# Kernel tuning notes

Hardware: AMD Instinct MI355X
Metric: run time of the kernel (lower is better)

The kernel has to match this reference:

```python
import jax, jax.numpy as jnp
import numpy as np

B, M, C = 8, 8192, 256   # batch, seeds, seed feature dim
F = 128                  # vote feature dim
P, K = 256, 32           # proposals, samples per group
CA, NCLS = 256, 10       # aggregated feat dim, classes
RADIUS = 0.3


def _lin(x, w, b):
    # 1x1 conv == pointwise linear; w: (out, in)
    return jnp.einsum('...c,oc->...o', x, w) + b


def _bnrelu(x, s, t):
    # eval-mode BatchNorm folded to per-channel affine, then ReLU
    return jnp.maximum(x * s + t, 0.0)


def _fps(xyz, npoint):
    # farthest point sampling; deterministic start at index 0
    Bb, N, _ = xyz.shape
    bidx = jnp.arange(Bb)

    def step(carry, _):
        distance, farthest = carry
        centroid = xyz[bidx, farthest][:, None, :]          # (B,1,2)
        d = jnp.sum((xyz - centroid) ** 2, -1)              # (B,N)
        distance = jnp.minimum(distance, d)
        return (distance, jnp.argmax(distance, -1)), farthest

    init = (jnp.full((Bb, N), 1e10, xyz.dtype), jnp.zeros((Bb,), jnp.int32))
    _, idx = jax.lax.scan(step, init, None, length=npoint)
    return jnp.transpose(idx)                               # (B, npoint)


def _ball_query(xyz, new_xyz, radius, nsample):
    # squared-distance cdist (monotone in euclid dist, so same sort order)
    N = xyz.shape[1]
    d2 = (jnp.sum(new_xyz ** 2, -1)[:, :, None]
          + jnp.sum(xyz ** 2, -1)[:, None, :]
          - 2.0 * jnp.einsum('bsd,bnd->bsn', new_xyz, xyz))  # (B,S,N)
    gidx = jnp.broadcast_to(jnp.arange(N), d2.shape)
    # out-of-radius points replaced by group_first (= index 0, as in source)
    gidx = jnp.where(d2 > radius * radius, 0, gidx)
    order = jnp.argsort(d2, axis=-1)
    return jnp.take_along_axis(gidx, order, axis=-1)[:, :, :nsample]


def _gather(points, idx):
    # points: (B,N,C); idx: (B,...) -> (B,...,C)
    return jax.vmap(lambda p, i: p[i])(points, idx)


def _forward(seed_xyz, seed_feats,
             v_off_w1, v_off_b1, v_off_s1, v_off_t1, v_off_w2, v_off_b2,
             v_ft_w1, v_ft_b1, v_ft_s1, v_ft_t1, v_ft_w2, v_ft_b2,
             a_w1, a_b1, a_s1, a_t1, a_w2, a_b2, a_s2, a_t2,
             p_w1, p_b1, p_s1, p_t1, p_w2, p_b2, p_s2, p_t2,
             obj_w, obj_b, cls_w, cls_b):
    # --- VotingModule (vote_factor=1) ---
    h = _bnrelu(_lin(seed_feats, v_off_w1, v_off_b1), v_off_s1, v_off_t1)
    offsets = _lin(h, v_off_w2, v_off_b2)                   # (B,M,2)
    g = _bnrelu(_lin(seed_feats, v_ft_w1, v_ft_b1), v_ft_s1, v_ft_t1)
    vote_feats = _lin(g, v_ft_w2, v_ft_b2)                  # (B,M,F)
    votes_xyz = seed_xyz + offsets                          # (B,M,2)

    # --- VoteAggregation ---
    fps_idx = _fps(votes_xyz, P)                            # (B,P)
    new_xyz = _gather(votes_xyz, fps_idx)                   # (B,P,2)
    gidx = _ball_query(votes_xyz, new_xyz, RADIUS, K)       # (B,P,K)
    gv = _gather(votes_xyz, gidx)                           # (B,P,K,2)
    gf = _gather(vote_feats, gidx)                          # (B,P,K,F)
    comb = jnp.concatenate([gv - new_xyz[:, :, None, :], gf], -1)  # (B,P,K,F+2)
    x = _bnrelu(_lin(comb, a_w1, a_b1), a_s1, a_t1)
    x = _bnrelu(_lin(x, a_w2, a_b2), a_s2, a_t2)
    pooled = jnp.max(x, axis=2)                             # (B,P,CA)

    # --- ProposalHead ---
    y = _bnrelu(_lin(pooled, p_w1, p_b1), p_s1, p_t1)
    y = _bnrelu(_lin(y, p_w2, p_b2), p_s2, p_t2)
    obj = _lin(y, obj_w, obj_b)[..., 0]                     # (B,P)
    cls = _lin(y, cls_w, cls_b)                             # (B,P,NCLS)
    return (new_xyz, obj, cls)


def setup_inputs() -> dict:
    key = jax.random.key(0)
    keys = iter(jax.random.split(key, 40))

    def w(shape):
        return (jax.random.normal(next(keys), shape) * 0.05).astype(jnp.float32)

    inp = {
        'seed_xyz': jax.random.uniform(next(keys), (B, M, 2), jnp.float32),
        'seed_feats': jax.random.normal(next(keys), (B, M, C), jnp.float32),
        # voting: offset branch
        'v_off_w1': w((C, C)), 'v_off_b1': w((C,)),
        'v_off_s1': 1.0 + w((C,)), 'v_off_t1': w((C,)),
        'v_off_w2': w((2, C)), 'v_off_b2': w((2,)),
        # voting: feature branch
        'v_ft_w1': w((C, C)), 'v_ft_b1': w((C,)),
        'v_ft_s1': 1.0 + w((C,)), 'v_ft_t1': w((C,)),
        'v_ft_w2': w((F, C)), 'v_ft_b2': w((F,)),
        # aggregation MLP
        'a_w1': w((CA, F + 2)), 'a_b1': w((CA,)),
        'a_s1': 1.0 + w((CA,)), 'a_t1': w((CA,)),
        'a_w2': w((CA, CA)), 'a_b2': w((CA,)),
        'a_s2': 1.0 + w((CA,)), 'a_t2': w((CA,)),
        # proposal head
        'p_w1': w((CA, CA)), 'p_b1': w((CA,)),
        'p_s1': 1.0 + w((CA,)), 'p_t1': w((CA,)),
        'p_w2': w((CA // 2, CA)), 'p_b2': w((CA // 2,)),
        'p_s2': 1.0 + w((CA // 2,)), 'p_t2': w((CA // 2,)),
        'obj_w': w((1, CA // 2)), 'obj_b': w((1,)),
        'cls_w': w((NCLS, CA // 2)), 'cls_b': w((NCLS,)),
    }
    return inp


def reference(seed_xyz, seed_feats,
              v_off_w1, v_off_b1, v_off_s1, v_off_t1, v_off_w2, v_off_b2,
              v_ft_w1, v_ft_b1, v_ft_s1, v_ft_t1, v_ft_w2, v_ft_b2,
              a_w1, a_b1, a_s1, a_t1, a_w2, a_b2, a_s2, a_t2,
              p_w1, p_b1, p_s1, p_t1, p_w2, p_b2, p_s2, p_t2,
              obj_w, obj_b, cls_w, cls_b):
    return _forward(seed_xyz, seed_feats,
                    v_off_w1, v_off_b1, v_off_s1, v_off_t1, v_off_w2, v_off_b2,
                    v_ft_w1, v_ft_b1, v_ft_s1, v_ft_t1, v_ft_w2, v_ft_b2,
                    a_w1, a_b1, a_s1, a_t1, a_w2, a_b2, a_s2, a_t2,
                    p_w1, p_b1, p_s1, p_t1, p_w2, p_b2, p_s2, p_t2,
                    obj_w, obj_b, cls_w, cls_b)
```

## Files before the change

### kernel.cpp

```cpp
#include <hip/hip_runtime.h>

typedef __attribute__((ext_vector_type(8))) short bf16x8;
typedef __attribute__((ext_vector_type(4))) float f32x4;
typedef unsigned short u16;
typedef unsigned int u32;
typedef unsigned long long u64;

#define DEV static __device__ __forceinline__
DEV u16 f2bf(float f) { u32 i = __float_as_uint(f); i += 0x7fffu + ((i >> 16) & 1u); return (u16)(i >> 16); }
DEV float bf2f(u16 u) { return __uint_as_float(((u32)u) << 16); }

constexpr int Mn = 8192;
constexpr int Pn = 256;
constexpr int Kn = 32;
constexpr float R2 = 0.09f;

__global__ __launch_bounds__(256, 2) void k_voting_off(
    const float* __restrict__ sxyz,
    const float* __restrict__ sfeat,
    const float* __restrict__ ow1, const float* __restrict__ ob1,
    const float* __restrict__ os1, const float* __restrict__ ot1,
    const float* __restrict__ ow2, const float* __restrict__ ob2,
    float* __restrict__ votes)
{
  __shared__ __align__(16) float Xc[16][34];
  __shared__ __align__(16) float Wc[16][262];
  __shared__ __align__(16) float Hst[256][33];

  const int tid = threadIdx.x;
  const int row0 = blockIdx.x * 32;

  const int wv = tid >> 6;
  const int w8 = wv * 8;
  const int cg = tid & 63;

  float acc[8][4];
#pragma unroll
  for (int r = 0; r < 8; ++r)
#pragma unroll
    for (int j = 0; j < 4; ++j) acc[r][j] = 0.f;

  for (int kc = 0; kc < 16; ++kc) {
    __syncthreads();
    for (int i = tid; i < 256 * 16; i += 256) {
      int o = i >> 4, k = i & 15;
      Wc[k][o] = ow1[o * 256 + kc * 16 + k];
    }
    for (int i = tid; i < 32 * 16; i += 256) {
      int r = i >> 4, k = i & 15;
      Xc[k][r] = sfeat[(row0 + r) * 256 + kc * 16 + k];
    }
    __syncthreads();
#pragma unroll
    for (int k = 0; k < 16; ++k) {
      float2 x01 = *(const float2*)&Xc[k][w8];
      float2 x23 = *(const float2*)&Xc[k][w8 + 2];
      float2 x45 = *(const float2*)&Xc[k][w8 + 4];
      float2 x67 = *(const float2*)&Xc[k][w8 + 6];
      float2 wlo = *(const float2*)&Wc[k][2 * cg];
      float2 whi = *(const float2*)&Wc[k][128 + 2 * cg];
      float x[8] = {x01.x, x01.y, x23.x, x23.y, x45.x, x45.y, x67.x, x67.y};
      float w[4] = {wlo.x, wlo.y, whi.x, whi.y};
#pragma unroll
      for (int r = 0; r < 8; ++r)
#pragma unroll
        for (int j = 0; j < 4; ++j)
          acc[r][j] = fmaf(x[r], w[j], acc[r][j]);
    }
  }
  __syncthreads();
#pragma unroll
  for (int j = 0; j < 4; ++j) {
    int o = (j < 2) ? (2 * cg + j) : (126 + 2 * cg + j);
    float bb = ob1[o], ss = os1[o], tt = ot1[o];
#pragma unroll
    for (int r = 0; r < 8; ++r)
      Hst[o][w8 + r] = fmaxf((acc[r][j] + bb) * ss + tt, 0.f);
  }
  __syncthreads();

  if (tid < 64) {
    int r = tid >> 1, o = tid & 1;
    float a = 0.f;
    for (int k = 0; k < 256; ++k)
      a = fmaf(Hst[k][r], ow2[o * 256 + k], a);
    a += ob2[o];
    int row = row0 + r;
    votes[row * 2 + o] = sxyz[row * 2 + o] + a;
  }
}

__global__ __launch_bounds__(512) void k_fps_vf(
    const float* __restrict__ votes, float* __restrict__ nxyz,
    float* __restrict__ out,
    const float* __restrict__ sfeat, const u16* __restrict__ FW1h,
    const float* __restrict__ fb1, const float* __restrict__ fs1,
    const float* __restrict__ ft1, const u16* __restrict__ FW2b,
    const float* __restrict__ fb2, u16* __restrict__ vfeat)
{
  __shared__ __align__(16) char smem[86016];
  const int tid = threadIdx.x;

  if (blockIdx.x < 8) {
    const int b = blockIdx.x;
    const float* vb = votes + b * Mn * 2;
    float2* xy   = (float2*)smem;
    u32*   Sd    = (u32*)(smem + 65536);
    u32*   Sl    = (u32*)(smem + 65536 + 256);
    float* histx = (float*)(smem + 66048);
    float* histy = (float*)(smem + 67072);

    {
      const float4* vb4 = (const float4*)vb;
#pragma unroll
      for (int j = tid; j < Mn / 2; j += 512) {
        float4 v = vb4[j];
        *(float4*)&xy[2 * j] = v;
      }
    }
    float dist[16];
#pragma unroll
    for (int s = 0; s < 16; ++s) dist[s] = 1e10f;
    __syncthreads();

    float cx = xy[0].x, cy = xy[0].y;
    if (tid == 0) { histx[0] = cx; histy[0] = cy; }

    for (int it = 1; it < Pn; ++it) {
      float bd = -1.f; int sb = 0;
#pragma unroll
      for (int s = 0; s < 16; ++s) {
        float2 p = xy[s * 512 + tid];
        float dx = p.x - cx, dy = p.y - cy;
        float d = fminf(dist[s], dx * dx + dy * dy);
        dist[s] = d;
        if (d > bd) { bd = d; sb = s; }
      }
      int bi = sb * 512 + tid;

      u32 hd = __float_as_uint(bd), hl = ~(u32)bi;

#define FPS_ROR(VD, VL, N)                                                      \
      {                                                                         \
        u32 od = (u32)__builtin_amdgcn_update_dpp(0, (int)VD, 0x120 + N, 0xF, 0xF, false); \
        u32 ol = (u32)__builtin_amdgcn_update_dpp(0, (int)VL, 0x120 + N, 0xF, 0xF, false); \
        bool g = (od > VD) || (od == VD && ol > VL);                            \
        VD = g ? od : VD; VL = g ? ol : VL;                                     \
      }
      FPS_ROR(hd, hl, 8)
      FPS_ROR(hd, hl, 4)
      FPS_ROR(hd, hl, 2)
      FPS_ROR(hd, hl, 1)

      const int buf = it & 1;
      if ((tid & 15) == 0) {
        int row = tid >> 4;
        Sd[buf * 32 + row] = hd; Sl[buf * 32 + row] = hl;
      }
      __syncthreads();

      int rr = tid & 15;
      u32 rd = Sd[buf * 32 + rr], rl = Sl[buf * 32 + rr];
      {
        u32 od = Sd[buf * 32 + 16 + rr], ol = Sl[buf * 32 + 16 + rr];
        bool g = (od > rd) || (od == rd && ol > rl);
        rd = g ? od : rd; rl = g ? ol : rl;
      }
      FPS_ROR(rd, rl, 8)
      FPS_ROR(rd, rl, 4)
      FPS_ROR(rd, rl, 2)
      FPS_ROR(rd, rl, 1)
#undef FPS_ROR

      int widx = (int)(~rl);
      float2 w = xy[widx];
      cx = w.x; cy = w.y;
      if (tid == 0) { histx[it] = cx; histy[it] = cy; }
    }
    __syncthreads();
    if (tid < 256) {
      float2 o2; o2.x = histx[tid]; o2.y = histy[tid];
      *(float2*)&nxyz[(b * Pn + tid) * 2] = o2;
      *(float2*)&out[(b * Pn + tid) * 2] = o2;
    }
  } else {
    const int bx = blockIdx.x - 8;
    const int row0 = bx * 128;
    u16* Hs = (u16*)smem;
    u16* As = (u16*)(smem + 34816);
    u16* Bs = (u16*)(smem + 45056);

    const int wid = tid >> 6, lane = tid & 63, m16 = lane & 15, quad = lane >> 4;
    const int wr = wid >> 2;
    const int wc4 = wid & 3;
    const int sr = tid >> 2, sk = (tid & 3) * 8;

    f32x4 acc2[4][2];
#pragma unroll
    for (int mt = 0; mt < 4; ++mt)
#pragma unroll
      for (int nt = 0; nt < 2; ++nt) acc2[mt][nt] = (f32x4){0.f, 0.f, 0.f, 0.f};

    for (int h = 0; h < 2; ++h) {
      f32x4 acc[4][2];
#pragma unroll
      for (int mt = 0; mt < 4; ++mt)
#pragma unroll
        for (int nt = 0; nt < 2; ++nt) acc[mt][nt] = (f32x4){0.f, 0.f, 0.f, 0.f};

      for (int s = 0; s < 8; ++s) {
        __syncthreads();
        {
          const float* src = &sfeat[(row0 + sr) * 256 + s * 32 + sk];
          float4 v0 = *(const float4*)&src[0];
          float4 v1 = *(const float4*)&src[4];
          u32 packed[4];
          packed[0] = (u32)f2bf(v0.x) | ((u32)f2bf(v0.y) << 16);
          packed[1] = (u32)f2bf(v0.z) | ((u32)f2bf(v0.w) << 16);
          packed[2] = (u32)f2bf(v1.x) | ((u32)f2bf(v1.y) << 16);
          packed[3] = (u32)f2bf(v1.z) | ((u32)f2bf(v1.w) << 16);
          *(uint4*)&As[sr * 40 + sk] = *(uint4*)&packed[0];
          *(uint4*)&Bs[sr * 40 + sk] =
              *(const uint4*)&FW1h[(h * 128 + sr) * 256 + s * 32 + sk];
        }
        __syncthreads();
#pragma unroll
        for (int mt = 0; mt < 4; ++mt) {
          bf16x8 af = *(const bf16x8*)&As[(wr * 64 + mt * 16 + m16) * 40 + quad * 8];
#pragma unroll
          for (int nt = 0; nt < 2; ++nt) {
            bf16x8 bfr = *(const bf16x8*)&Bs[(wc4 * 32 + nt * 16 + m16) * 40 + quad * 8];
            acc[mt][nt] = __builtin_amdgcn_mfma_f32_16x16x32_bf16(af, bfr, acc[mt][nt], 0, 0, 0);
          }
        }
      }
      __syncthreads();
#pragma unroll
      for (int nt = 0; nt < 2; ++nt) {
        int colL = wc4 * 32 + nt * 16 + m16;
        int col = h * 128 + colL;
        float bb = fb1[col], ss = fs1[col], tt = ft1[col];
#pragma unroll
        for (int mt = 0; mt < 4; ++mt) {
          int rL = wr * 64 + mt * 16 + quad * 4;
#pragma unroll
          for (int r = 0; r < 4; ++r)
            Hs[(rL + r) * 136 + colL] = f2bf(fmaxf((acc[mt][nt][r] + bb) * ss + tt, 0.f));
        }
      }
      for (int s2 = 0; s2 < 4; ++s2) {
        __syncthreads();
        {
          *(uint4*)&Bs[sr * 40 + sk] =
              *(const uint4*)&FW2b[sr * 256 + h * 128 + s2 * 32 + sk];
        }
        __syncthreads();
#pragma unroll
        for (int mt = 0; mt < 4; ++mt) {
          bf16x8 af = *(const bf16x8*)&Hs[(wr * 64 + mt * 16 + m16) * 136 + s2 * 32 + quad * 8];
#pragma unroll
          for (int nt = 0; nt < 2; ++nt) {
            bf16x8 bfr = *(const bf16x8*)&Bs[(wc4 * 32 + nt * 16 + m16) * 40 + quad * 8];
            acc2[mt][nt] = __builtin_amdgcn_mfma_f32_16x16x32_bf16(af, bfr, acc2[mt][nt], 0, 0, 0);
          }
        }
      }
    }
#pragma unroll
    for (int nt = 0; nt < 2; ++nt) {
      int col = wc4 * 32 + nt * 16 + m16;
      float bb = fb2[col];
#pragma unroll
      for (int mt = 0; mt < 4; ++mt) {
        int rbase = row0 + wr * 64 + mt * 16 + quad * 4;
#pragma unroll
        for (int r = 0; r < 4; ++r)
          vfeat[(rbase + r) * 128 + col] = f2bf(acc2[mt][nt][r] + bb);
      }
    }
  }
}

__global__ __launch_bounds__(256) void k_ballq(
    const float* __restrict__ votes, const float* __restrict__ nxyz,
    int* __restrict__ gidx)
{
  const int bp = blockIdx.x, tid = threadIdx.x;
  const int b = bp >> 8;
  const float* vb = votes + b * Mn * 2;
  const float sx = nxyz[bp * 2], sy = nxyz[bp * 2 + 1];
  const float a = sx * sx + sy * sy;
  float d2[32];
#pragma unroll
  for (int s = 0; s < 32; ++s) {
    int i = tid * 32 + s;
    float x = vb[i * 2], y = vb[i * 2 + 1];
    d2[s] = (a + (x * x + y * y)) - 2.f * (sx * x + sy * y);
  }
  __shared__ float sd[4];
  __shared__ int si[4];
  __shared__ int swi;
  unsigned mask = 0;
  for (int kk = 0; kk < Kn; ++kk) {
    float bd = 3.4e38f; int bi = 0x7fffffff;
#pragma unroll
    for (int s = 0; s < 32; ++s)
      if (!((mask >> s) & 1u) && d2[s] < bd) { bd = d2[s]; bi = tid * 32 + s; }
#pragma unroll
    for (int off = 32; off > 0; off >>= 1) {
      float od = __shfl_xor(bd, off);
      int oi = __shfl_xor(bi, off);
      if (od < bd || (od == bd && oi < bi)) { bd = od; bi = oi; }
    }
    if ((tid & 63) == 0) { sd[tid >> 6] = bd; si[tid >> 6] = bi; }
    __syncthreads();
    if (tid == 0) {
#pragma unroll
      for (int w = 1; w < 4; ++w)
        if (sd[w] < bd || (sd[w] == bd && si[w] < bi)) { bd = sd[w]; bi = si[w]; }
      swi = bi;
      gidx[bp * Kn + kk] = (bd > R2) ? 0 : bi;
    }
    __syncthreads();
    int wi = swi;
    if ((wi >> 5) == tid) mask |= 1u << (wi & 31);
  }
}

__global__ __launch_bounds__(256) void k_prep(
    const float* __restrict__ fw1, const float* __restrict__ fw2,
    const float* __restrict__ aw1, const float* __restrict__ aw2,
    u16* __restrict__ FW1h, u16* __restrict__ FW2b,
    u16* __restrict__ AW1b, u16* __restrict__ AW2b)
{
  const int gid = blockIdx.x * 256 + threadIdx.x;
  const int gsz = gridDim.x * 256;
  for (int i = gid; i < 65536; i += gsz) FW1h[i] = f2bf(fw1[i]);
  for (int i = gid; i < 32768; i += gsz) FW2b[i] = f2bf(fw2[i]);
  for (int i = gid; i < 65536; i += gsz) AW2b[i] = f2bf(aw2[i]);
  for (int i = gid; i < 49152; i += gsz) {
    int o = i / 192, k = i % 192;
    AW1b[i] = (k < 130) ? f2bf(aw1[o * 130 + k]) : (u16)0;
  }
}

__global__ __launch_bounds__(256) void k_agg(
    const float* __restrict__ votes, const u16* __restrict__ vfeat,
    const float* __restrict__ nxyz, const int* __restrict__ gidx,
    const u16* __restrict__ AW1b, const float* __restrict__ ab1,
    const float* __restrict__ as1, const float* __restrict__ at1,
    const u16* __restrict__ AW2b, const float* __restrict__ ab2,
    const float* __restrict__ as2, const float* __restrict__ at2,
    float* __restrict__ pooled)
{
  __shared__ u16 U[32 * 264];
  __shared__ u16 Bs[256 * 72];
  __shared__ int gix[32];
  __shared__ float gvx[32], gvy[32];
  u16* CombA = U;
  u16* As = U;
  float* x2T = (float*)Bs;

  const int bp = blockIdx.x, tid = threadIdx.x, b = bp >> 8;
  if (tid < 32) {
    int g = gidx[bp * 32 + tid];
    gix[tid] = g;
    gvx[tid] = votes[(b * Mn + g) * 2];
    gvy[tid] = votes[(b * Mn + g) * 2 + 1];
  }
  __syncthreads();
  const float sx = nxyz[bp * 2], sy = nxyz[bp * 2 + 1];

  if (tid < 192) {
    int row = tid / 6, c = tid % 6;
    const u16* vsrc = &vfeat[(b * Mn + gix[row]) * 128];
    u16* dst = &CombA[row * 200 + c * 32];
    if (c == 0) {
      dst[0] = f2bf(gvx[row] - sx);
      dst[1] = f2bf(gvy[row] - sy);
      for (int k = 2; k < 32; ++k) dst[k] = vsrc[k - 2];
    } else if (c <= 3) {
      for (int k = 0; k < 32; ++k) dst[k] = vsrc[c * 32 + k - 2];
    } else if (c == 4) {
      dst[0] = vsrc[126]; dst[1] = vsrc[127];
      for (int k = 2; k < 32; ++k) dst[k] = 0;
    } else {
      for (int k = 0; k < 32; ++k) dst[k] = 0;
    }
  }

  const int wid = tid >> 6, lane = tid & 63, m16 = lane & 15, quad = lane >> 4;
  const int mt = wid & 1, nh = wid >> 1;

  f32x4 acc[8];
#pragma unroll
  for (int nt = 0; nt < 8; ++nt) acc[nt] = (f32x4){0.f, 0.f, 0.f, 0.f};
  for (int s = 0; s < 3; ++s) {
    __syncthreads();
    for (int i = tid; i < 4096; i += 256) {
      int n = i >> 4, c4 = i & 15;
      *(uint2*)&Bs[n * 72 + c4 * 4] = *(const uint2*)&AW1b[n * 192 + s * 64 + c4 * 4];
    }
    __syncthreads();
#pragma unroll
    for (int ks = 0; ks < 2; ++ks) {
      bf16x8 af = *(const bf16x8*)&CombA[(mt * 16 + m16) * 200 + s * 64 + ks * 32 + quad * 8];
#pragma unroll
      for (int nt = 0; nt < 8; ++nt) {
        bf16x8 bf_ = *(const bf16x8*)&Bs[(nh * 128 + nt * 16 + m16) * 72 + ks * 32 + quad * 8];
        acc[nt] = __builtin_amdgcn_mfma_f32_16x16x32_bf16(af, bf_, acc[nt], 0, 0, 0);
      }
    }
  }
  __syncthreads();
#pragma unroll
  for (int nt = 0; nt < 8; ++nt) {
    int col = nh * 128 + nt * 16 + m16;
    float bb = ab1[col], ss = as1[col], tt = at1[col];
#pragma unroll
    for (int r = 0; r < 4; ++r) {
      int samp = mt * 16 + quad * 4 + r;
      As[samp * 264 + col] = f2bf(fmaxf((acc[nt][r] + bb) * ss + tt, 0.f));
    }
  }

  f32x4 acc2[8];
#pragma unroll
  for (int nt = 0; nt < 8; ++nt) acc2[nt] = (f32x4){0.f, 0.f, 0.f, 0.f};
  for (int s = 0; s < 4; ++s) {
    __syncthreads();
    for (int i = tid; i < 4096; i += 256) {
      int n = i >> 4, c4 = i & 15;
      *(uint2*)&Bs[n * 72 + c4 * 4] = *(const uint2*)&AW2b[n * 256 + s * 64 + c4 * 4];
    }
    __syncthreads();
#pragma unroll
    for (int ks = 0; ks < 2; ++ks) {
      bf16x8 af = *(const bf16x8*)&As[(mt * 16 + m16) * 264 + s * 64 + ks * 32 + quad * 8];
#pragma unroll
      for (int nt = 0; nt < 8; ++nt) {
        bf16x8 bf_ = *(const bf16x8*)&Bs[(nh * 128 + nt * 16 + m16) * 72 + ks * 32 + quad * 8];
        acc2[nt] = __builtin_amdgcn_mfma_f32_16x16x32_bf16(af, bf_, acc2[nt], 0, 0, 0);
      }
    }
  }
  __syncthreads();
#pragma unroll
  for (int nt = 0; nt < 8; ++nt) {
    int col = nh * 128 + nt * 16 + m16;
    float bb = ab2[col], ss = as2[col], tt = at2[col];
#pragma unroll
    for (int r = 0; r < 4; ++r) {
      int samp = mt * 16 + quad * 4 + r;
      x2T[col * 33 + samp] = fmaxf((acc2[nt][r] + bb) * ss + tt, 0.f);
    }
  }
  __syncthreads();
  {
    float m = x2T[tid * 33];
#pragma unroll
    for (int s2 = 1; s2 < 32; ++s2) m = fmaxf(m, x2T[tid * 33 + s2]);
    pooled[bp * 256 + tid] = m;
  }
}

__global__ __launch_bounds__(256) void k_head(
    const float* __restrict__ pooled,
    const float* __restrict__ pw1, const float* __restrict__ pb1,
    const float* __restrict__ ps1, const float* __restrict__ pt1,
    const float* __restrict__ pw2, const float* __restrict__ pb2,
    const float* __restrict__ ps2, const float* __restrict__ pt2,
    const float* __restrict__ objw, const float* __restrict__ objb,
    const float* __restrict__ clsw, const float* __restrict__ clsb,
    float* __restrict__ out)
{
  __shared__ float xr[256], y1[256], y2[128];
  const int bp = blockIdx.x, tid = threadIdx.x;
  xr[tid] = pooled[bp * 256 + tid];
  __syncthreads();
  {
    float a = 0.f;
    for (int c = 0; c < 256; ++c) a = fmaf(xr[c], pw1[tid * 256 + c], a);
    a = (a + pb1[tid]) * ps1[tid] + pt1[tid];
    y1[tid] = fmaxf(a, 0.f);
  }
  __syncthreads();
  if (tid < 128) {
    float a = 0.f;
    for (int c = 0; c < 256; ++c) a = fmaf(y1[c], pw2[tid * 256 + c], a);
    a = (a + pb2[tid]) * ps2[tid] + pt2[tid];
    y2[tid] = fmaxf(a, 0.f);
  }
  __syncthreads();
  if (tid < 10) {
    float a = 0.f;
    for (int c = 0; c < 128; ++c) a = fmaf(y2[c], clsw[tid * 128 + c], a);
    out[6144 + bp * 10 + tid] = a + clsb[tid];
  } else if (tid == 10) {
    float a = 0.f;
    for (int c = 0; c < 128; ++c) a = fmaf(y2[c], objw[c], a);
    out[4096 + bp] = a + objb[0];
  }
}

extern "C" void kernel_launch(void* const* d_in, const int* in_sizes, int n_in,
                              void* d_out, int out_size, void* d_ws, size_t ws_size,
                              hipStream_t stream)
{
  (void)in_sizes; (void)n_in; (void)out_size; (void)ws_size;
  const float* sxyz  = (const float*)d_in[0];
  const float* sfeat = (const float*)d_in[1];
  const float* ow1 = (const float*)d_in[2];
  const float* ob1 = (const float*)d_in[3];
  const float* os1 = (const float*)d_in[4];
  const float* ot1 = (const float*)d_in[5];
  const float* ow2 = (const float*)d_in[6];
  const float* ob2 = (const float*)d_in[7];
  const float* fw1 = (const float*)d_in[8];
  const float* fb1 = (const float*)d_in[9];
  const float* fs1 = (const float*)d_in[10];
  const float* ft1 = (const float*)d_in[11];
  const float* fw2 = (const float*)d_in[12];
  const float* fb2 = (const float*)d_in[13];
  const float* aw1 = (const float*)d_in[14];
  const float* ab1 = (const float*)d_in[15];
  const float* as1 = (const float*)d_in[16];
  const float* at1 = (const float*)d_in[17];
  const float* aw2 = (const float*)d_in[18];
  const float* ab2 = (const float*)d_in[19];
  const float* as2 = (const float*)d_in[20];
  const float* at2 = (const float*)d_in[21];
  const float* pw1 = (const float*)d_in[22];
  const float* pb1 = (const float*)d_in[23];
  const float* ps1 = (const float*)d_in[24];
  const float* pt1 = (const float*)d_in[25];
  const float* pw2 = (const float*)d_in[26];
  const float* pb2 = (const float*)d_in[27];
  const float* ps2 = (const float*)d_in[28];
  const float* pt2 = (const float*)d_in[29];
  const float* objw = (const float*)d_in[30];
  const float* objb = (const float*)d_in[31];
  const float* clsw = (const float*)d_in[32];
  const float* clsb = (const float*)d_in[33];

  char* ws = (char*)d_ws;
  float* votes  = (float*)(ws + 0);
  u16*   vfeat  = (u16*)  (ws + 524288);
  float* nxyz   = (float*)(ws + 17301504);
  int*   gidxp  = (int*)  (ws + 17317888);
  float* pooled = (float*)(ws + 17580032);
  u16*   FW1h   = (u16*)  (ws + 19677184);
  u16*   FW2b   = (u16*)  (ws + 19808256);
  u16*   AW1b   = (u16*)  (ws + 19873792);
  u16*   AW2b   = (u16*)  (ws + 19972096);
  float* out    = (float*)d_out;

  k_prep<<<dim3(256), dim3(256), 0, stream>>>(
      fw1, fw2, aw1, aw2, FW1h, FW2b, AW1b, AW2b);

  k_voting_off<<<dim3(2048), dim3(256), 0, stream>>>(
      sxyz, sfeat, ow1, ob1, os1, ot1, ow2, ob2, votes);

  k_fps_vf<<<dim3(520), dim3(512), 0, stream>>>(
      votes, nxyz, out,
      sfeat, FW1h, fb1, fs1, ft1, FW2b, fb2, vfeat);

  k_ballq<<<dim3(2048), dim3(256), 0, stream>>>(votes, nxyz, gidxp);

  k_agg<<<dim3(2048), dim3(256), 0, stream>>>(
      votes, vfeat, nxyz, gidxp, AW1b, ab1, as1, at1,
      AW2b, ab2, as2, at2, pooled);

  k_head<<<dim3(2048), dim3(256), 0, stream>>>(
      pooled, pw1, pb1, ps1, pt1, pw2, pb2, ps2, pt2,
      objw, objb, clsw, clsb, out);
}
```

Measured before the change: 891.1 us.

## Retile voting offset GEMM to 64 rows and fuse aggregation with proposal head

The voting-offset kernel now processes 64 rows per block with an 8x8 register tile and float4 shared loads, halving the grid and raising arithmetic intensity per shared load. The Hst buffer is aliased over the X/W staging area, which puts the kernel at about 67 KB of shared memory per block. The proposal head is merged into the aggregation kernel, so pooled features stay in shared memory instead of going through global memory and a separate launch. The risks are lower occupancy from the larger shared footprint and register tile, and a longer serial tail in the fused kernel.

Measured after the change: 854.9 us. 4.1% less time.

```diff
diff --git a/kernel.cpp b/kernel.cpp
--- a/kernel.cpp
+++ b/kernel.cpp
@@ -23,22 +23,22 @@
     const float* __restrict__ ow2, const float* __restrict__ ob2,
     float* __restrict__ votes)
 {
-  __shared__ __align__(16) float Xc[16][34];
-  __shared__ __align__(16) float Wc[16][262];
-  __shared__ __align__(16) float Hst[256][33];
+  __shared__ __align__(16) char vsm[68608];
+  float (*Xc)[68]  = (float(*)[68])vsm;
+  float (*Wc)[260] = (float(*)[260])(vsm + 4352);
+  float (*Hst)[67] = (float(*)[67])vsm;
 
   const int tid = threadIdx.x;
-  const int row0 = blockIdx.x * 32;
-
-  const int wv = tid >> 6;
-  const int w8 = wv * 8;
-  const int cg = tid & 63;
-
-  float acc[8][4];
+  const int row0 = blockIdx.x * 64;
+  const int wv = tid >> 6, lane = tid & 63;
+  const int rr = wv * 16 + (lane >> 5) * 8;
+  const int c4 = (lane & 31) * 4;
+
+  float acc[8][8];
 #pragma unroll
   for (int r = 0; r < 8; ++r)
 #pragma unroll
-    for (int j = 0; j < 4; ++j) acc[r][j] = 0.f;
+    for (int j = 0; j < 8; ++j) acc[r][j] = 0.f;
 
   for (int kc = 0; kc < 16; ++kc) {
     __syncthreads();
@@ -46,40 +46,38 @@
       int o = i >> 4, k = i & 15;
       Wc[k][o] = ow1[o * 256 + kc * 16 + k];
     }
-    for (int i = tid; i < 32 * 16; i += 256) {
+    for (int i = tid; i < 64 * 16; i += 256) {
       int r = i >> 4, k = i & 15;
       Xc[k][r] = sfeat[(row0 + r) * 256 + kc * 16 + k];
     }
     __syncthreads();
 #pragma unroll
     for (int k = 0; k < 16; ++k) {
-      float2 x01 = *(const float2*)&Xc[k][w8];
-      float2 x23 = *(const float2*)&Xc[k][w8 + 2];
-      float2 x45 = *(const float2*)&Xc[k][w8 + 4];
-      float2 x67 = *(const float2*)&Xc[k][w8 + 6];
-      float2 wlo = *(const float2*)&Wc[k][2 * cg];
-      float2 whi = *(const float2*)&Wc[k][128 + 2 * cg];
-      float x[8] = {x01.x, x01.y, x23.x, x23.y, x45.x, x45.y, x67.x, x67.y};
-      float w[4] = {wlo.x, wlo.y, whi.x, whi.y};
+      float4 x0 = *(const float4*)&Xc[k][rr];
+      float4 x1 = *(const float4*)&Xc[k][rr + 4];
+      float4 w0 = *(const float4*)&Wc[k][c4];
+      float4 w1 = *(const float4*)&Wc[k][128 + c4];
+      float x[8] = {x0.x, x0.y, x0.z, x0.w, x1.x, x1.y, x1.z, x1.w};
+      float w[8] = {w0.x, w0.y, w0.z, w0.w, w1.x, w1.y, w1.z, w1.w};
 #pragma unroll
       for (int r = 0; r < 8; ++r)
 #pragma unroll
-        for (int j = 0; j < 4; ++j)
+        for (int j = 0; j < 8; ++j)
           acc[r][j] = fmaf(x[r], w[j], acc[r][j]);
     }
   }
   __syncthreads();
 #pragma unroll
-  for (int j = 0; j < 4; ++j) {
-    int o = (j < 2) ? (2 * cg + j) : (126 + 2 * cg + j);
+  for (int j = 0; j < 8; ++j) {
+    int o = (j < 4) ? (c4 + j) : (124 + c4 + j);
     float bb = ob1[o], ss = os1[o], tt = ot1[o];
 #pragma unroll
     for (int r = 0; r < 8; ++r)
-      Hst[o][w8 + r] = fmaxf((acc[r][j] + bb) * ss + tt, 0.f);
-  }
-  __syncthreads();
-
-  if (tid < 64) {
+      Hst[o][rr + r] = fmaxf((acc[r][j] + bb) * ss + tt, 0.f);
+  }
+  __syncthreads();
+
+  if (tid < 128) {
     int r = tid >> 1, o = tid & 1;
     float a = 0.f;
     for (int k = 0; k < 256; ++k)
@@ -344,14 +342,20 @@
   }
 }
 
-__global__ __launch_bounds__(256) void k_agg(
+__global__ __launch_bounds__(256) void k_agg_head(
     const float* __restrict__ votes, const u16* __restrict__ vfeat,
     const float* __restrict__ nxyz, const int* __restrict__ gidx,
     const u16* __restrict__ AW1b, const float* __restrict__ ab1,
     const float* __restrict__ as1, const float* __restrict__ at1,
     const u16* __restrict__ AW2b, const float* __restrict__ ab2,
     const float* __restrict__ as2, const float* __restrict__ at2,
-    float* __restrict__ pooled)
+    const float* __restrict__ pw1, const float* __restrict__ pb1,
+    const float* __restrict__ ps1, const float* __restrict__ pt1,
+    const float* __restrict__ pw2, const float* __restrict__ pb2,
+    const float* __restrict__ ps2, const float* __restrict__ pt2,
+    const float* __restrict__ objw, const float* __restrict__ objb,
+    const float* __restrict__ clsw, const float* __restrict__ clsb,
+    float* __restrict__ out)
 {
   __shared__ u16 U[32 * 264];
   __shared__ u16 Bs[256 * 72];
@@ -360,6 +364,9 @@
   u16* CombA = U;
   u16* As = U;
   float* x2T = (float*)Bs;
+  float* xr = (float*)U;
+  float* y1 = ((float*)U) + 256;
+  float* y2 = ((float*)U) + 512;
 
   const int bp = blockIdx.x, tid = threadIdx.x, b = bp >> 8;
   if (tid < 32) {
@@ -460,24 +467,10 @@
     float m = x2T[tid * 33];
 #pragma unroll
     for (int s2 = 1; s2 < 32; ++s2) m = fmaxf(m, x2T[tid * 33 + s2]);
-    pooled[bp * 256 + tid] = m;
-  }
-}
-
-__global__ __launch_bounds__(256) void k_head(
-    const float* __restrict__ pooled,
-    const float* __restrict__ pw1, const float* __restrict__ pb1,
-    const float* __restrict__ ps1, const float* __restrict__ pt1,
-    const float* __restrict__ pw2, const float* __restrict__ pb2,
-    const float* __restrict__ ps2, const float* __restrict__ pt2,
-    const float* __restrict__ objw, const float* __restrict__ objb,
-    const float* __restrict__ clsw, const float* __restrict__ clsb,
-    float* __restrict__ out)
-{
-  __shared__ float xr[256], y1[256], y2[128];
-  const int bp = blockIdx.x, tid = threadIdx.x;
-  xr[tid] = pooled[bp * 256 + tid];
-  __syncthreads();
+    xr[tid] = m;
+  }
+  __syncthreads();
+
   {
     float a = 0.f;
     for (int c = 0; c < 256; ++c) a = fmaf(xr[c], pw1[tid * 256 + c], a);
@@ -548,7 +541,6 @@
   u16*   vfeat  = (u16*)  (ws + 524288);
   float* nxyz   = (float*)(ws + 17301504);
   int*   gidxp  = (int*)  (ws + 17317888);
-  float* pooled = (float*)(ws + 17580032);
   u16*   FW1h   = (u16*)  (ws + 19677184);
   u16*   FW2b   = (u16*)  (ws + 19808256);
   u16*   AW1b   = (u16*)  (ws + 19873792);
@@ -558,7 +550,7 @@
   k_prep<<<dim3(256), dim3(256), 0, stream>>>(
       fw1, fw2, aw1, aw2, FW1h, FW2b, AW1b, AW2b);
 
-  k_voting_off<<<dim3(2048), dim3(256), 0, stream>>>(
+  k_voting_off<<<dim3(1024), dim3(256), 0, stream>>>(
       sxyz, sfeat, ow1, ob1, os1, ot1, ow2, ob2, votes);
 
   k_fps_vf<<<dim3(520), dim3(512), 0, stream>>>(
@@ -567,11 +559,9 @@
 
   k_ballq<<<dim3(2048), dim3(256), 0, stream>>>(votes, nxyz, gidxp);
 
-  k_agg<<<dim3(2048), dim3(256), 0, stream>>>(
+  k_agg_head<<<dim3(2048), dim3(256), 0, stream>>>(
       votes, vfeat, nxyz, gidxp, AW1b, ab1, as1, at1,
-      AW2b, ab2, as2, at2, pooled);
-
-  k_head<<<dim3(2048), dim3(256), 0, stream>>>(
-      pooled, pw1, pb1, ps1, pt1, pw2, pb2, ps2, pt2,
+      AW2b, ab2, as2, at2,
+      pw1, pb1, ps1, pt1, pw2, pb2, ps2, pt2,
       objw, objb, clsw, clsb, out);
 }
```
